# Performance work log

Measured on AMD Instinct MI355X. Metric: run time of the kernel, lower is better.

The kernel has to match this reference:

```python
import jax, jax.numpy as jnp
import numpy as np

N_SAMPLING = 32
N_FINAL = 8
FEATURE_DEPTH = 128
H = 128
W = 128
N_LINES = 50000


def setup_inputs() -> dict:
    key = jax.random.key(0)
    k1, k2 = jax.random.split(key)
    features_per_image = jax.random.normal(k1, (FEATURE_DEPTH, H, W), dtype=jnp.float32)
    # line endpoints in pixel coordinates, roughly spanning the feature map
    lines_per_im = jax.random.uniform(k2, (N_LINES, 4), dtype=jnp.float32) * float(W)
    return {"features_per_image": features_per_image, "lines_per_im": lines_per_im}


def reference(features_per_image, lines_per_im):
    C, h, w = features_per_image.shape
    tspan = jnp.linspace(0.0, 1.0, N_SAMPLING, dtype=jnp.float32)[None, None, :]  # [1,1,S]
    U = lines_per_im[:, :2]   # [N,2]
    V = lines_per_im[:, 2:]   # [N,2]
    # [N,2,S] -> permute -> [N*S, 2]
    sampled = U[:, :, None] * tspan + V[:, :, None] * (1.0 - tspan) - 0.5
    sampled = jnp.transpose(sampled, (0, 2, 1)).reshape(-1, 2)
    px, py = sampled[:, 0], sampled[:, 1]
    px0 = jnp.clip(jnp.floor(px), 0.0, w - 1)
    py0 = jnp.clip(jnp.floor(py), 0.0, h - 1)
    px1 = jnp.clip(px0 + 1.0, 0.0, w - 1)
    py1 = jnp.clip(py0 + 1.0, 0.0, h - 1)
    px0l, py0l = px0.astype(jnp.int32), py0.astype(jnp.int32)
    px1l, py1l = px1.astype(jnp.int32), py1.astype(jnp.int32)
    # four bilinear gathers, each [C, N*S]
    xp = (features_per_image[:, py0l, px0l] * ((py1 - py) * (px1 - px))[None, :]
          + features_per_image[:, py1l, px0l] * ((py - py0) * (px1 - px))[None, :]
          + features_per_image[:, py0l, px1l] * ((py1 - py) * (px - px0))[None, :]
          + features_per_image[:, py1l, px1l] * ((py - py0) * (px - px0))[None, :])
    # [C, N, S] -> [N, C, S]
    xp = jnp.transpose(xp.reshape(C, -1, N_SAMPLING), (1, 0, 2))
    # MaxPool1d(kernel=stride=S//F): [N, C, F, S//F] -> max over last axis
    pool = N_SAMPLING // N_FINAL
    xp = xp.reshape(xp.shape[0], C, N_FINAL, pool).max(axis=-1)
    return xp.reshape(-1, N_FINAL * FEATURE_DEPTH)
```

## Files before the change

kernel.cpp:

```cpp
#include <hip/hip_runtime.h>
#include <hip/hip_fp16.h>
#include <float.h>

#define C_DEPTH 128
#define H_DIM 128
#define W_DIM 128
#define NPIX (H_DIM * W_DIM)
#define N_SAMP 32
#define N_FINAL 8
#define N_LINES 50000

typedef float v4f __attribute__((ext_vector_type(4)));

__global__ __launch_bounds__(256) void transpose_chw_hwc(
    const float* __restrict__ in, __half* __restrict__ out) {
    __shared__ float tile[64 * 129];
    const int p0 = blockIdx.x * 64;
    const int t = threadIdx.x;

    const int p_local = t & 63;
    const int cg = t >> 6;
    #pragma unroll
    for (int i = 0; i < 32; ++i) {
        const int ch = cg * 32 + i;
        tile[p_local * 129 + ch] = in[ch * NPIX + p0 + p_local];
    }
    __syncthreads();

    const int ch = t & 127;
    const int pg = t >> 7;
    #pragma unroll
    for (int i = 0; i < 32; ++i) {
        const int p = pg * 32 + i;
        out[(p0 + p) * C_DEPTH + ch] = __float2half(tile[p * 129 + ch]);
    }
}

__global__ __launch_bounds__(128) void line_pool(
    const __half* __restrict__ ft,
    const float* __restrict__ lines,
    float* __restrict__ out) {
    __shared__ int4   s_off[N_SAMP];
    __shared__ float4 s_w[N_SAMP];
    __shared__ float  o_tile[C_DEPTH * 9];

    const int line = blockIdx.x;
    const int t = threadIdx.x;

    if (t < N_SAMP) {
        const float4 l = reinterpret_cast<const float4*>(lines)[line];
        const float ts = (float)t / 31.0f;
        const float px = l.x * ts + l.z * (1.0f - ts) - 0.5f;
        const float py = l.y * ts + l.w * (1.0f - ts) - 0.5f;
        const float px0 = fminf(fmaxf(floorf(px), 0.0f), (float)(W_DIM - 1));
        const float py0 = fminf(fmaxf(floorf(py), 0.0f), (float)(H_DIM - 1));
        const float px1 = fminf(px0 + 1.0f, (float)(W_DIM - 1));
        const float py1 = fminf(py0 + 1.0f, (float)(H_DIM - 1));
        const int ix0 = (int)px0, iy0 = (int)py0;
        const int ix1 = (int)px1, iy1 = (int)py1;
        const float wx0 = px1 - px, wx1 = px - px0;
        const float wy0 = py1 - py, wy1 = py - py0;
        s_off[t] = make_int4((iy0 * W_DIM + ix0) * C_DEPTH,
                             (iy1 * W_DIM + ix0) * C_DEPTH,
                             (iy0 * W_DIM + ix1) * C_DEPTH,
                             (iy1 * W_DIM + ix1) * C_DEPTH);
        s_w[t] = make_float4(wy0 * wx0, wy1 * wx0, wy0 * wx1, wy1 * wx1);
    }
    __syncthreads();

    const int f  = t >> 4;
    const int tg = t & 15;
    const int c0 = tg * 8;

    float acc[8];
    #pragma unroll
    for (int j = 0; j < 8; ++j) acc[j] = -FLT_MAX;

    #pragma unroll
    for (int si = 0; si < 4; ++si) {
        const int s = f * 4 + si;
        const int4   o  = s_off[s];
        const float4 wv = s_w[s];
        const float4 r00 = *reinterpret_cast<const float4*>(ft + o.x + c0);
        const float4 r10 = *reinterpret_cast<const float4*>(ft + o.y + c0);
        const float4 r01 = *reinterpret_cast<const float4*>(ft + o.z + c0);
        const float4 r11 = *reinterpret_cast<const float4*>(ft + o.w + c0);
        const __half2* h00 = reinterpret_cast<const __half2*>(&r00);
        const __half2* h10 = reinterpret_cast<const __half2*>(&r10);
        const __half2* h01 = reinterpret_cast<const __half2*>(&r01);
        const __half2* h11 = reinterpret_cast<const __half2*>(&r11);
        #pragma unroll
        for (int k = 0; k < 4; ++k) {
            const float2 f00 = __half22float2(h00[k]);
            const float2 f10 = __half22float2(h10[k]);
            const float2 f01 = __half22float2(h01[k]);
            const float2 f11 = __half22float2(h11[k]);
            const float vx = f00.x * wv.x + f10.x * wv.y + f01.x * wv.z + f11.x * wv.w;
            const float vy = f00.y * wv.x + f10.y * wv.y + f01.y * wv.z + f11.y * wv.w;
            acc[2 * k]     = fmaxf(acc[2 * k],     vx);
            acc[2 * k + 1] = fmaxf(acc[2 * k + 1], vy);
        }
    }

    #pragma unroll
    for (int j = 0; j < 8; ++j) o_tile[(c0 + j) * 9 + f] = acc[j];
    __syncthreads();

    float* op = out + (size_t)line * (C_DEPTH * N_FINAL) + t * N_FINAL;
    const float* row = &o_tile[t * 9];
    const v4f w0 = {row[0], row[1], row[2], row[3]};
    const v4f w1 = {row[4], row[5], row[6], row[7]};
    __builtin_nontemporal_store(w0, reinterpret_cast<v4f*>(op));
    __builtin_nontemporal_store(w1, reinterpret_cast<v4f*>(op) + 1);
}

extern "C" void kernel_launch(void* const* d_in, const int* in_sizes, int n_in,
                              void* d_out, int out_size, void* d_ws, size_t ws_size,
                              hipStream_t stream) {
    const float* feat  = (const float*)d_in[0];
    const float* lines = (const float*)d_in[1];
    float* out = (float*)d_out;
    __half* ft = (__half*)d_ws;

    transpose_chw_hwc<<<NPIX / 64, 256, 0, stream>>>(feat, ft);
    line_pool<<<N_LINES, 128, 0, stream>>>(ft, lines, out);
}
```

Measured before the change: 272.4 us.

## Split line pooling into two channel-half passes with per-wave line ownership

```diff
diff --git a/kernel.cpp b/kernel.cpp
--- a/kernel.cpp
+++ b/kernel.cpp
@@ -9,12 +9,14 @@
 #define N_SAMP 32
 #define N_FINAL 8
 #define N_LINES 50000
+#define C_HALF 64
+#define LPB 2
 
 typedef float v4f __attribute__((ext_vector_type(4)));
 
 __global__ __launch_bounds__(256) void transpose_chw_hwc(
     const float* __restrict__ in, __half* __restrict__ out) {
-    __shared__ float tile[64 * 129];
+    __shared__ float tile[64 * 130];
     const int p0 = blockIdx.x * 64;
     const int t = threadIdx.x;
 
@@ -23,33 +25,44 @@
     #pragma unroll
     for (int i = 0; i < 32; ++i) {
         const int ch = cg * 32 + i;
-        tile[p_local * 129 + ch] = in[ch * NPIX + p0 + p_local];
+        tile[p_local * 130 + ch] = in[ch * NPIX + p0 + p_local];
     }
     __syncthreads();
 
-    const int ch = t & 127;
-    const int pg = t >> 7;
+    const int cp = (t & 63) * 2;
+    const int pg = t >> 6;
     #pragma unroll
-    for (int i = 0; i < 32; ++i) {
-        const int p = pg * 32 + i;
-        out[(p0 + p) * C_DEPTH + ch] = __float2half(tile[p * 129 + ch]);
+    for (int i = 0; i < 16; ++i) {
+        const int p = pg * 16 + i;
+        const float2 f2 = *reinterpret_cast<const float2*>(&tile[p * 130 + cp]);
+        *reinterpret_cast<__half2*>(&out[(size_t)(p0 + p) * C_DEPTH + cp]) =
+            __floats2half2_rn(f2.x, f2.y);
     }
 }
 
-__global__ __launch_bounds__(128) void line_pool(
+__global__ __launch_bounds__(128) void line_pool_half(
     const __half* __restrict__ ft,
     const float* __restrict__ lines,
-    float* __restrict__ out) {
-    __shared__ int4   s_off[N_SAMP];
-    __shared__ float4 s_w[N_SAMP];
-    __shared__ float  o_tile[C_DEPTH * 9];
+    float* __restrict__ out,
+    const int c_base) {
+    __shared__ float o_tile[LPB][C_HALF * 9];
 
-    const int line = blockIdx.x;
-    const int t = threadIdx.x;
+    const int wid  = threadIdx.x >> 6;
+    const int lane = threadIdx.x & 63;
+    const int line = blockIdx.x * LPB + wid;
 
-    if (t < N_SAMP) {
-        const float4 l = reinterpret_cast<const float4*>(lines)[line];
-        const float ts = (float)t / 31.0f;
+    const int f  = lane >> 3;
+    const int tg = lane & 7;
+    const int c0 = c_base + tg * 8;
+
+    const float4 l = reinterpret_cast<const float4*>(lines)[line];
+
+    int4   o[4];
+    float4 w[4];
+    #pragma unroll
+    for (int si = 0; si < 4; ++si) {
+        const int s = f * 4 + si;
+        const float ts = (float)s / 31.0f;
         const float px = l.x * ts + l.z * (1.0f - ts) - 0.5f;
         const float py = l.y * ts + l.w * (1.0f - ts) - 0.5f;
         const float px0 = fminf(fmaxf(floorf(px), 0.0f), (float)(W_DIM - 1));
@@ -60,17 +73,21 @@
         const int ix1 = (int)px1, iy1 = (int)py1;
         const float wx0 = px1 - px, wx1 = px - px0;
         const float wy0 = py1 - py, wy1 = py - py0;
-        s_off[t] = make_int4((iy0 * W_DIM + ix0) * C_DEPTH,
-                             (iy1 * W_DIM + ix0) * C_DEPTH,
-                             (iy0 * W_DIM + ix1) * C_DEPTH,
-                             (iy1 * W_DIM + ix1) * C_DEPTH);
-        s_w[t] = make_float4(wy0 * wx0, wy1 * wx0, wy0 * wx1, wy1 * wx1);
+        o[si] = make_int4((iy0 * W_DIM + ix0) * C_DEPTH,
+                          (iy1 * W_DIM + ix0) * C_DEPTH,
+                          (iy0 * W_DIM + ix1) * C_DEPTH,
+                          (iy1 * W_DIM + ix1) * C_DEPTH);
+        w[si] = make_float4(wy0 * wx0, wy1 * wx0, wy0 * wx1, wy1 * wx1);
     }
-    __syncthreads();
 
-    const int f  = t >> 4;
-    const int tg = t & 15;
-    const int c0 = tg * 8;
+    float4 r[16];
+    #pragma unroll
+    for (int si = 0; si < 4; ++si) {
+        r[si * 4 + 0] = *reinterpret_cast<const float4*>(ft + o[si].x + c0);
+        r[si * 4 + 1] = *reinterpret_cast<const float4*>(ft + o[si].y + c0);
+        r[si * 4 + 2] = *reinterpret_cast<const float4*>(ft + o[si].z + c0);
+        r[si * 4 + 3] = *reinterpret_cast<const float4*>(ft + o[si].w + c0);
+    }
 
     float acc[8];
     #pragma unroll
@@ -78,17 +95,11 @@
 
     #pragma unroll
     for (int si = 0; si < 4; ++si) {
-        const int s = f * 4 + si;
-        const int4   o  = s_off[s];
-        const float4 wv = s_w[s];
-        const float4 r00 = *reinterpret_cast<const float4*>(ft + o.x + c0);
-        const float4 r10 = *reinterpret_cast<const float4*>(ft + o.y + c0);
-        const float4 r01 = *reinterpret_cast<const float4*>(ft + o.z + c0);
-        const float4 r11 = *reinterpret_cast<const float4*>(ft + o.w + c0);
-        const __half2* h00 = reinterpret_cast<const __half2*>(&r00);
-        const __half2* h10 = reinterpret_cast<const __half2*>(&r10);
-        const __half2* h01 = reinterpret_cast<const __half2*>(&r01);
-        const __half2* h11 = reinterpret_cast<const __half2*>(&r11);
+        const float4 wv = w[si];
+        const __half2* h00 = reinterpret_cast<const __half2*>(&r[si * 4 + 0]);
+        const __half2* h10 = reinterpret_cast<const __half2*>(&r[si * 4 + 1]);
+        const __half2* h01 = reinterpret_cast<const __half2*>(&r[si * 4 + 2]);
+        const __half2* h11 = reinterpret_cast<const __half2*>(&r[si * 4 + 3]);
         #pragma unroll
         for (int k = 0; k < 4; ++k) {
             const float2 f00 = __half22float2(h00[k]);
@@ -102,12 +113,14 @@
         }
     }
 
+    float* tl = o_tile[wid];
     #pragma unroll
-    for (int j = 0; j < 8; ++j) o_tile[(c0 + j) * 9 + f] = acc[j];
+    for (int j = 0; j < 8; ++j) tl[(tg * 8 + j) * 9 + f] = acc[j];
     __syncthreads();
 
-    float* op = out + (size_t)line * (C_DEPTH * N_FINAL) + t * N_FINAL;
-    const float* row = &o_tile[t * 9];
+    float* op = out + (size_t)line * (C_DEPTH * N_FINAL)
+                    + (size_t)(c_base + lane) * N_FINAL;
+    const float* row = &tl[lane * 9];
     const v4f w0 = {row[0], row[1], row[2], row[3]};
     const v4f w1 = {row[4], row[5], row[6], row[7]};
     __builtin_nontemporal_store(w0, reinterpret_cast<v4f*>(op));
@@ -123,5 +136,6 @@
     __half* ft = (__half*)d_ws;
 
     transpose_chw_hwc<<<NPIX / 64, 256, 0, stream>>>(feat, ft);
-    line_pool<<<N_LINES, 128, 0, stream>>>(ft, lines, out);
+    line_pool_half<<<N_LINES / LPB, 128, 0, stream>>>(ft, lines, out, 0);
+    line_pool_half<<<N_LINES / LPB, 128, 0, stream>>>(ft, lines, out, C_HALF);
 }
```

New measurement: 294.2 us. 8.0% more time.
